# Optimization experiments

Hardware: AMD Instinct MI355X
Metric: run time of the kernel (lower is better)

Reference implementation:

```python
import jax, jax.numpy as jnp
import numpy as np

ALPHA = 0.2   # LeakyReLU negative slope
EPS = 1e-8
N_NODES = 100000
N_EDGES = 1600000
D_IN = 128
D_OUT = 128


def setup_inputs() -> dict:
    key = jax.random.key(0)
    k1, k2, k3, k4, k5 = jax.random.split(key, 5)
    h = jax.random.normal(k1, (N_NODES, D_IN), dtype=jnp.float32)
    edge_index = jax.random.randint(k2, (2, N_EDGES), 0, N_NODES, dtype=jnp.int32)
    edge_weight = jax.random.uniform(k3, (N_EDGES,), dtype=jnp.float32)
    # xavier-ish scaled params
    W = jax.random.normal(k4, (D_OUT, D_IN), dtype=jnp.float32) * (1.0 / np.sqrt(D_IN))
    a = jax.random.normal(k5, (1, 2 * D_OUT), dtype=jnp.float32) * (1.0 / np.sqrt(2 * D_OUT))
    return {"h": h, "edge_index": edge_index, "edge_weight": edge_weight, "W": W, "a": a}


def reference(h, edge_index, edge_weight, W, a):
    num_nodes = h.shape[0]
    Wh = h @ W.T                                   # [N, D_OUT]
    src, dst = edge_index[0], edge_index[1]
    d_out = Wh.shape[1]
    a_src = a[0, :d_out]                           # a^T [Wh_i || Wh_j] split into two dots
    a_dst = a[0, d_out:]
    Wh_src = Wh[src]                               # [E, D_OUT] edge gather
    e = Wh_src @ a_src + Wh[dst] @ a_dst           # [E]
    e = jnp.where(e >= 0, e, ALPHA * e)            # LeakyReLU
    e = e * edge_weight
    # segment softmax over edges sharing dst; torch init-to-zero amax => max(seg_max, 0)
    seg_max = jax.ops.segment_max(e, dst, num_segments=num_nodes)
    seg_max = jnp.maximum(seg_max, 0.0)
    ex = jnp.exp(e - seg_max[dst])
    seg_sum = jax.ops.segment_sum(ex, dst, num_segments=num_nodes)
    att = ex / (seg_sum[dst] + EPS)                # [E]
    # weighted scatter-add aggregation (dropout is identity in eval/p=0)
    h_prime = jax.ops.segment_sum(att[:, None] * Wh_src, dst, num_segments=num_nodes)
    return h_prime
```

## Files before the change

### kernel.cpp

```cpp
#include <hip/hip_runtime.h>
#include <hip/hip_bf16.h>
#include <math.h>

#define D_FEAT 128
#define ALPHA 0.2f
#define EPS 1e-8f

#define BSHIFT 7
#define BNODES 128
#define NB_MAX 800
#define NB_PAD 1024
#define CAP_B 2432
#define CCHUNK 2048

typedef __bf16 bf16x8 __attribute__((ext_vector_type(8)));
typedef float f32x4 __attribute__((ext_vector_type(4)));

__device__ __forceinline__ void split_bf16(const float* __restrict__ p,
                                           bf16x8& hi, bf16x8& lo)
{
    f32x4 a = *(const f32x4*)p;
    f32x4 b = *(const f32x4*)(p + 4);
#pragma unroll
    for (int j = 0; j < 4; ++j) {
        float x = a[j]; __bf16 xh = (__bf16)x;
        hi[j] = xh; lo[j] = (__bf16)(x - (float)xh);
        float y = b[j]; __bf16 yh = (__bf16)y;
        hi[j + 4] = yh; lo[j + 4] = (__bf16)(y - (float)yh);
    }
}

__global__ __launch_bounds__(256) void presplit_w(
    const float* __restrict__ W, __bf16* __restrict__ Whi, __bf16* __restrict__ Wlo)
{
    const int i = blockIdx.x * 256 + threadIdx.x;
    const float x = W[i];
    const __bf16 xh = (__bf16)x;
    Whi[i] = xh;
    Wlo[i] = (__bf16)(x - (float)xh);
}

__global__ __launch_bounds__(256) void gemm_s_kernel(
    const float* __restrict__ h,
    const __bf16* __restrict__ Whi, const __bf16* __restrict__ Wlo,
    const float* __restrict__ a, __bf16* __restrict__ Whb,
    float* __restrict__ s_src, float* __restrict__ s_dst, int N)
{
    const int wave = threadIdx.x >> 6;
    const int lane = threadIdx.x & 63;
    const int row0 = blockIdx.x * 128 + wave * 32;
    if (row0 >= N) return;

    const int l15 = lane & 15;
    const int quad = lane >> 4;

    bf16x8 ahi[2][4], alo[2][4];
#pragma unroll
    for (int m = 0; m < 2; ++m) {
        int arow = row0 + m * 16 + l15;
        if (arow >= N) arow = N - 1;
#pragma unroll
        for (int kk = 0; kk < 4; ++kk)
            split_bf16(h + (size_t)arow * D_FEAT + kk * 32 + quad * 8,
                       ahi[m][kk], alo[m][kk]);
    }

    f32x4 acc[2][8];
#pragma unroll
    for (int m = 0; m < 2; ++m)
#pragma unroll
        for (int n = 0; n < 8; ++n) acc[m][n] = (f32x4){0.f, 0.f, 0.f, 0.f};

#pragma unroll
    for (int kk = 0; kk < 4; ++kk) {
#pragma unroll
        for (int n = 0; n < 8; ++n) {
            const size_t boff = (size_t)(n * 16 + l15) * D_FEAT + kk * 32 + quad * 8;
            const bf16x8 bhi = *(const bf16x8*)(Whi + boff);
            const bf16x8 blo = *(const bf16x8*)(Wlo + boff);
#pragma unroll
            for (int m = 0; m < 2; ++m) {
                acc[m][n] = __builtin_amdgcn_mfma_f32_16x16x32_bf16(ahi[m][kk], bhi, acc[m][n], 0, 0, 0);
                acc[m][n] = __builtin_amdgcn_mfma_f32_16x16x32_bf16(ahi[m][kk], blo, acc[m][n], 0, 0, 0);
                acc[m][n] = __builtin_amdgcn_mfma_f32_16x16x32_bf16(alo[m][kk], bhi, acc[m][n], 0, 0, 0);
            }
        }
    }

#pragma unroll
    for (int m = 0; m < 2; ++m) {
        const int rbase = row0 + m * 16;
        float psrc[4] = {0.f, 0.f, 0.f, 0.f};
        float pdst[4] = {0.f, 0.f, 0.f, 0.f};
#pragma unroll
        for (int n = 0; n < 8; ++n) {
            const int col = n * 16 + l15;
            const float as = a[col];
            const float ad = a[D_FEAT + col];
#pragma unroll
            for (int r = 0; r < 4; ++r) {
                const int row = rbase + quad * 4 + r;
                const float v = acc[m][n][r];
                if (row < N) Whb[(size_t)row * D_FEAT + col] = (__bf16)v;
                psrc[r] += v * as;
                pdst[r] += v * ad;
            }
        }
#pragma unroll
        for (int off = 1; off < 16; off <<= 1) {
#pragma unroll
            for (int r = 0; r < 4; ++r) {
                psrc[r] += __shfl_xor(psrc[r], off, 64);
                pdst[r] += __shfl_xor(pdst[r], off, 64);
            }
        }
        if (l15 == 0) {
#pragma unroll
            for (int r = 0; r < 4; ++r) {
                const int row = rbase + quad * 4 + r;
                if (row < N) { s_src[row] = psrc[r]; s_dst[row] = pdst[r]; }
            }
        }
    }
}

__global__ __launch_bounds__(256) void bin_sort_local(
    const int* __restrict__ src, const int* __restrict__ dst,
    const float* __restrict__ ew,
    const float* __restrict__ s_src, const float* __restrict__ s_dst,
    int* __restrict__ gcur, uint2* __restrict__ bin, int E, int NB)
{
    __shared__ uint2 srt[CCHUNK];
    __shared__ unsigned short sbkt[CCHUNK];
    __shared__ int lhist[NB_PAD];
    __shared__ int loff[NB_PAD];
    __shared__ int lcur[NB_PAD];
    __shared__ int gbase[NB_PAD];
    __shared__ int sh[256];

    const int t = threadIdx.x;
    const int i0 = blockIdx.x * CCHUNK + t * 8;

    lhist[t] = 0; lhist[t + 256] = 0; lhist[t + 512] = 0; lhist[t + 768] = 0;
    __syncthreads();

    int n = E - i0; n = n < 0 ? 0 : (n > 8 ? 8 : n);
    int ss[8], dd[8];
    float wwv[8], exv[8];
    unsigned meta[8];
    int bb[8];

    if (n == 8) {
        const int4 sa = *(const int4*)(src + i0);
        const int4 sb = *(const int4*)(src + i0 + 4);
        const int4 da = *(const int4*)(dst + i0);
        const int4 db = *(const int4*)(dst + i0 + 4);
        const float4 wa = *(const float4*)(ew + i0);
        const float4 wb = *(const float4*)(ew + i0 + 4);
        ss[0] = sa.x; ss[1] = sa.y; ss[2] = sa.z; ss[3] = sa.w;
        ss[4] = sb.x; ss[5] = sb.y; ss[6] = sb.z; ss[7] = sb.w;
        dd[0] = da.x; dd[1] = da.y; dd[2] = da.z; dd[3] = da.w;
        dd[4] = db.x; dd[5] = db.y; dd[6] = db.z; dd[7] = db.w;
        wwv[0] = wa.x; wwv[1] = wa.y; wwv[2] = wa.z; wwv[3] = wa.w;
        wwv[4] = wb.x; wwv[5] = wb.y; wwv[6] = wb.z; wwv[7] = wb.w;
    } else {
        for (int k = 0; k < n; ++k) {
            ss[k] = src[i0 + k]; dd[k] = dst[i0 + k]; wwv[k] = ew[i0 + k];
        }
    }
#pragma unroll
    for (int k = 0; k < 8; ++k) {
        if (k < n) {
            const int s = ss[k], d = dd[k];
            float e = s_src[s] + s_dst[d];
            e = (e >= 0.f) ? e : ALPHA * e;
            e *= wwv[k];
            exv[k] = expf(e);
            bb[k] = d >> BSHIFT;
            meta[k] = (unsigned)s | ((unsigned)(d & (BNODES - 1)) << 17);
            atomicAdd(&lhist[bb[k]], 1);
        }
    }
    __syncthreads();

    const int v0 = lhist[4 * t];
    const int v1 = lhist[4 * t + 1];
    const int v2 = lhist[4 * t + 2];
    const int v3 = lhist[4 * t + 3];
    const int ts = v0 + v1 + v2 + v3;
    sh[t] = ts;
    __syncthreads();
    for (int off = 1; off < 256; off <<= 1) {
        int x = (t >= off) ? sh[t - off] : 0;
        __syncthreads();
        sh[t] += x;
        __syncthreads();
    }
    int run = sh[t] - ts;
    loff[4 * t] = run;     lcur[4 * t] = run;     run += v0;
    loff[4 * t + 1] = run; lcur[4 * t + 1] = run; run += v1;
    loff[4 * t + 2] = run; lcur[4 * t + 2] = run; run += v2;
    loff[4 * t + 3] = run; lcur[4 * t + 3] = run;
    const int total = sh[255];

    for (int b = t; b < NB; b += 256) {
        const int c = lhist[b];
        gbase[b] = c ? atomicAdd(&gcur[b], c) : 0;
    }
    __syncthreads();

#pragma unroll
    for (int k = 0; k < 8; ++k) {
        if (k < n) {
            const int p = atomicAdd(&lcur[bb[k]], 1);
            srt[p] = make_uint2(meta[k], __float_as_uint(exv[k]));
            sbkt[p] = (unsigned short)bb[k];
        }
    }
    __syncthreads();

    for (int i = t; i < total; i += 256) {
        const int b = sbkt[i];
        const int gpos = gbase[b] + (i - loff[b]);
        if (gpos < CAP_B)
            bin[(size_t)b * CAP_B + gpos] = srt[i];
    }
}

__global__ __launch_bounds__(512) void sort_aggregate(
    const int* __restrict__ gcur, const uint2* __restrict__ bin,
    const __bf16* __restrict__ Whb, float* __restrict__ out, int N)
{
    __shared__ uint2 srec[CAP_B];
    __shared__ float ssums[BNODES];
    __shared__ int lhist[BNODES];
    __shared__ int loff[BNODES];
    __shared__ int lcur[BNODES];
    __shared__ int sh[BNODES];

    const int t = threadIdx.x;
    const int b = blockIdx.x;
    const size_t base = (size_t)b * CAP_B;
    const int node0 = b << BSHIFT;
    const int nnodes = min(BNODES, N - node0);
    int cnt = gcur[b];
    if (cnt > CAP_B) cnt = CAP_B;

    if (t < BNODES) { lhist[t] = 0; ssums[t] = 0.f; }
    __syncthreads();

    for (int i = t; i < cnt; i += 512)
        atomicAdd(&lhist[(bin[base + i].x >> 17) & (BNODES - 1)], 1);
    __syncthreads();

    int hv = 0;
    if (t < BNODES) { hv = lhist[t]; sh[t] = hv; }
    __syncthreads();
    for (int off = 1; off < BNODES; off <<= 1) {
        int x = (t >= off && t < BNODES) ? sh[t - off] : 0;
        __syncthreads();
        if (t < BNODES) sh[t] += x;
        __syncthreads();
    }
    if (t < BNODES) { loff[t] = sh[t] - hv; lcur[t] = sh[t] - hv; }
    __syncthreads();

    for (int i = t; i < cnt; i += 512) {
        const uint2 r = bin[base + i];
        const unsigned dl = (r.x >> 17) & (BNODES - 1);
        const int p = atomicAdd(&lcur[dl], 1);
        srec[p] = make_uint2(r.x & 0x1FFFFu, r.y);
        atomicAdd(&ssums[dl], __uint_as_float(r.y));
    }
    __syncthreads();

    const int wave = t >> 6;
    const int lane = t & 63;
    const int quad = lane >> 4;
    const int c0 = (lane & 15) * 8;

    for (int nd = wave; nd < nnodes; nd += 8) {
        const int rb = loff[nd];
        const int cnt_n = lhist[nd];
        const float inv = 1.f / (ssums[nd] + EPS);

        float acc[8];
#pragma unroll
        for (int i = 0; i < 8; ++i) acc[i] = 0.f;

        int j = 0;
        for (; j + 15 < cnt_n; j += 16) {
            uint2 m[4];
#pragma unroll
            for (int g = 0; g < 4; ++g) m[g] = srec[rb + j + g * 4 + quad];
            bf16x8 v[4];
#pragma unroll
            for (int g = 0; g < 4; ++g)
                v[g] = *(const bf16x8*)(Whb + (size_t)m[g].x * D_FEAT + c0);
#pragma unroll
            for (int g = 0; g < 4; ++g) {
                const float a0 = __uint_as_float(m[g].y);
#pragma unroll
                for (int i = 0; i < 8; ++i) acc[i] += a0 * (float)v[g][i];
            }
        }
        for (; j + 7 < cnt_n; j += 8) {
            const uint2 m0 = srec[rb + j + quad];
            const uint2 m1 = srec[rb + j + 4 + quad];
            const float a0 = __uint_as_float(m0.y);
            const float a1 = __uint_as_float(m1.y);
            const bf16x8 v0 = *(const bf16x8*)(Whb + (size_t)m0.x * D_FEAT + c0);
            const bf16x8 v1 = *(const bf16x8*)(Whb + (size_t)m1.x * D_FEAT + c0);
#pragma unroll
            for (int i = 0; i < 8; ++i)
                acc[i] += a0 * (float)v0[i] + a1 * (float)v1[i];
        }
        for (; j < cnt_n; j += 4) {
            const int je = j + quad;
            const int jc = je < cnt_n ? je : cnt_n - 1;
            const uint2 m = srec[rb + jc];
            const float a0 = (je < cnt_n) ? __uint_as_float(m.y) : 0.f;
            const bf16x8 v = *(const bf16x8*)(Whb + (size_t)m.x * D_FEAT + c0);
#pragma unroll
            for (int i = 0; i < 8; ++i) acc[i] += a0 * (float)v[i];
        }
#pragma unroll
        for (int i = 0; i < 8; ++i) {
            acc[i] += __shfl_xor(acc[i], 16, 64);
            acc[i] += __shfl_xor(acc[i], 32, 64);
            acc[i] *= inv;
        }
        if (lane < 16) {
            f32x4 r0, r1;
            r0[0] = acc[0]; r0[1] = acc[1]; r0[2] = acc[2]; r0[3] = acc[3];
            r1[0] = acc[4]; r1[1] = acc[5]; r1[2] = acc[6]; r1[3] = acc[7];
            float* po = out + (size_t)(node0 + nd) * D_FEAT + c0;
            *(f32x4*)po = r0;
            *(f32x4*)(po + 4) = r1;
        }
    }
}

extern "C" void kernel_launch(void* const* d_in, const int* in_sizes, int n_in,
                              void* d_out, int out_size, void* d_ws, size_t ws_size,
                              hipStream_t stream) {
    const float* h  = (const float*)d_in[0];
    const int* eidx = (const int*)d_in[1];
    const float* ew = (const float*)d_in[2];
    const float* W  = (const float*)d_in[3];
    const float* a  = (const float*)d_in[4];
    float* out      = (float*)d_out;

    const int N = in_sizes[0] / D_FEAT;
    const int E = in_sizes[2];
    const int* src = eidx;
    const int* dst = eidx + E;

    const int NB = (N + BNODES - 1) / BNODES;

    char* ws = (char*)d_ws;
    size_t off = 0;
    int*    gcur      = (int*)(ws + off);   off += (size_t)NB_MAX * 4;
    float*  s_src     = (float*)(ws + off); off += (size_t)N * 4;
    float*  s_dst     = (float*)(ws + off); off += (size_t)N * 4;
    off = (off + 15) & ~(size_t)15;
    __bf16* Whi       = (__bf16*)(ws + off); off += (size_t)D_FEAT * D_FEAT * 2;
    __bf16* Wlo       = (__bf16*)(ws + off); off += (size_t)D_FEAT * D_FEAT * 2;
    uint2*  bin       = (uint2*)(ws + off);  off += (size_t)NB_MAX * CAP_B * 8;
    __bf16* Whb       = (__bf16*)(ws + off); off += (size_t)N * D_FEAT * 2;

    hipMemsetAsync(gcur, 0, (size_t)NB * 4, stream);

    presplit_w<<<64, 256, 0, stream>>>(W, Whi, Wlo);
    gemm_s_kernel<<<(N + 127) / 128, 256, 0, stream>>>(h, Whi, Wlo, a, Whb, s_src, s_dst, N);
    bin_sort_local<<<(E + CCHUNK - 1) / CCHUNK, 256, 0, stream>>>(
        src, dst, ew, s_src, s_dst, gcur, bin, E, NB);
    sort_aggregate<<<NB, 512, 0, stream>>>(gcur, bin, Whb, out, N);
}
```

Before: 270.5 us.

## Store Wh as fp16, fold memset into presplit, widen bin sort blocks

Several changes at once. Wh is stored as fp16 instead of bf16, trading range for mantissa accuracy at the same bandwidth. The gcur memset is folded into the presplit_w kernel to save a launch. bin_sort_local now uses 512 threads over 4096-edge chunks and __expf instead of expf. In sort_aggregate, per-node softmax sums are computed by a wave reduction over sorted records rather than shared-memory float atomics. fp16 could overflow for large Wh values, and the larger sort chunk raises LDS use and lowers the block count.

```diff
diff --git a/kernel.cpp b/kernel.cpp
--- a/kernel.cpp
+++ b/kernel.cpp
@@ -11,9 +11,10 @@
 #define NB_MAX 800
 #define NB_PAD 1024
 #define CAP_B 2432
-#define CCHUNK 2048
+#define CCHUNK 4096
 
 typedef __bf16 bf16x8 __attribute__((ext_vector_type(8)));
+typedef _Float16 f16x8 __attribute__((ext_vector_type(8)));
 typedef float f32x4 __attribute__((ext_vector_type(4)));
 
 __device__ __forceinline__ void split_bf16(const float* __restrict__ p,
@@ -31,19 +32,23 @@
 }
 
 __global__ __launch_bounds__(256) void presplit_w(
-    const float* __restrict__ W, __bf16* __restrict__ Whi, __bf16* __restrict__ Wlo)
+    const float* __restrict__ W, __bf16* __restrict__ Whi, __bf16* __restrict__ Wlo,
+    int* __restrict__ gcur)
 {
     const int i = blockIdx.x * 256 + threadIdx.x;
     const float x = W[i];
     const __bf16 xh = (__bf16)x;
     Whi[i] = xh;
     Wlo[i] = (__bf16)(x - (float)xh);
+    if (blockIdx.x == 0) {
+        for (int b = threadIdx.x; b < NB_MAX; b += 256) gcur[b] = 0;
+    }
 }
 
 __global__ __launch_bounds__(256) void gemm_s_kernel(
     const float* __restrict__ h,
     const __bf16* __restrict__ Whi, const __bf16* __restrict__ Wlo,
-    const float* __restrict__ a, __bf16* __restrict__ Whb,
+    const float* __restrict__ a, _Float16* __restrict__ Whf,
     float* __restrict__ s_src, float* __restrict__ s_dst, int N)
 {
     const int wave = threadIdx.x >> 6;
@@ -101,7 +106,7 @@
             for (int r = 0; r < 4; ++r) {
                 const int row = rbase + quad * 4 + r;
                 const float v = acc[m][n][r];
-                if (row < N) Whb[(size_t)row * D_FEAT + col] = (__bf16)v;
+                if (row < N) Whf[(size_t)row * D_FEAT + col] = (_Float16)v;
                 psrc[r] += v * as;
                 pdst[r] += v * ad;
             }
@@ -124,7 +129,7 @@
     }
 }
 
-__global__ __launch_bounds__(256) void bin_sort_local(
+__global__ __launch_bounds__(512) void bin_sort_local(
     const int* __restrict__ src, const int* __restrict__ dst,
     const float* __restrict__ ew,
     const float* __restrict__ s_src, const float* __restrict__ s_dst,
@@ -136,12 +141,12 @@
     __shared__ int loff[NB_PAD];
     __shared__ int lcur[NB_PAD];
     __shared__ int gbase[NB_PAD];
-    __shared__ int sh[256];
+    __shared__ int sh[512];
 
     const int t = threadIdx.x;
     const int i0 = blockIdx.x * CCHUNK + t * 8;
 
-    lhist[t] = 0; lhist[t + 256] = 0; lhist[t + 512] = 0; lhist[t + 768] = 0;
+    lhist[t] = 0; lhist[t + 512] = 0;
     __syncthreads();
 
     int n = E - i0; n = n < 0 ? 0 : (n > 8 ? 8 : n);
@@ -175,7 +180,7 @@
             float e = s_src[s] + s_dst[d];
             e = (e >= 0.f) ? e : ALPHA * e;
             e *= wwv[k];
-            exv[k] = expf(e);
+            exv[k] = __expf(e);
             bb[k] = d >> BSHIFT;
             meta[k] = (unsigned)s | ((unsigned)(d & (BNODES - 1)) << 17);
             atomicAdd(&lhist[bb[k]], 1);
@@ -183,27 +188,23 @@
     }
     __syncthreads();
 
-    const int v0 = lhist[4 * t];
-    const int v1 = lhist[4 * t + 1];
-    const int v2 = lhist[4 * t + 2];
-    const int v3 = lhist[4 * t + 3];
-    const int ts = v0 + v1 + v2 + v3;
+    const int v0 = lhist[2 * t];
+    const int v1 = lhist[2 * t + 1];
+    const int ts = v0 + v1;
     sh[t] = ts;
     __syncthreads();
-    for (int off = 1; off < 256; off <<= 1) {
+    for (int off = 1; off < 512; off <<= 1) {
         int x = (t >= off) ? sh[t - off] : 0;
         __syncthreads();
         sh[t] += x;
         __syncthreads();
     }
     int run = sh[t] - ts;
-    loff[4 * t] = run;     lcur[4 * t] = run;     run += v0;
-    loff[4 * t + 1] = run; lcur[4 * t + 1] = run; run += v1;
-    loff[4 * t + 2] = run; lcur[4 * t + 2] = run; run += v2;
-    loff[4 * t + 3] = run; lcur[4 * t + 3] = run;
-    const int total = sh[255];
-
-    for (int b = t; b < NB; b += 256) {
+    loff[2 * t] = run;     lcur[2 * t] = run;     run += v0;
+    loff[2 * t + 1] = run; lcur[2 * t + 1] = run;
+    const int total = sh[511];
+
+    for (int b = t; b < NB; b += 512) {
         const int c = lhist[b];
         gbase[b] = c ? atomicAdd(&gcur[b], c) : 0;
     }
@@ -219,7 +220,7 @@
     }
     __syncthreads();
 
-    for (int i = t; i < total; i += 256) {
+    for (int i = t; i < total; i += 512) {
         const int b = sbkt[i];
         const int gpos = gbase[b] + (i - loff[b]);
         if (gpos < CAP_B)
@@ -229,10 +230,9 @@
 
 __global__ __launch_bounds__(512) void sort_aggregate(
     const int* __restrict__ gcur, const uint2* __restrict__ bin,
-    const __bf16* __restrict__ Whb, float* __restrict__ out, int N)
+    const _Float16* __restrict__ Whf, float* __restrict__ out, int N)
 {
     __shared__ uint2 srec[CAP_B];
-    __shared__ float ssums[BNODES];
     __shared__ int lhist[BNODES];
     __shared__ int loff[BNODES];
     __shared__ int lcur[BNODES];
@@ -246,7 +246,7 @@
     int cnt = gcur[b];
     if (cnt > CAP_B) cnt = CAP_B;
 
-    if (t < BNODES) { lhist[t] = 0; ssums[t] = 0.f; }
+    if (t < BNODES) lhist[t] = 0;
     __syncthreads();
 
     for (int i = t; i < cnt; i += 512)
@@ -270,7 +270,6 @@
         const unsigned dl = (r.x >> 17) & (BNODES - 1);
         const int p = atomicAdd(&lcur[dl], 1);
         srec[p] = make_uint2(r.x & 0x1FFFFu, r.y);
-        atomicAdd(&ssums[dl], __uint_as_float(r.y));
     }
     __syncthreads();
 
@@ -282,7 +281,14 @@
     for (int nd = wave; nd < nnodes; nd += 8) {
         const int rb = loff[nd];
         const int cnt_n = lhist[nd];
-        const float inv = 1.f / (ssums[nd] + EPS);
+
+        float ssum = 0.f;
+        for (int jj = lane; jj < cnt_n; jj += 64)
+            ssum += __uint_as_float(srec[rb + jj].y);
+#pragma unroll
+        for (int off = 1; off < 64; off <<= 1)
+            ssum += __shfl_xor(ssum, off, 64);
+        const float inv = 1.f / (ssum + EPS);
 
         float acc[8];
 #pragma unroll
@@ -293,10 +299,10 @@
             uint2 m[4];
 #pragma unroll
             for (int g = 0; g < 4; ++g) m[g] = srec[rb + j + g * 4 + quad];
-            bf16x8 v[4];
+            f16x8 v[4];
 #pragma unroll
             for (int g = 0; g < 4; ++g)
-                v[g] = *(const bf16x8*)(Whb + (size_t)m[g].x * D_FEAT + c0);
+                v[g] = *(const f16x8*)(Whf + (size_t)m[g].x * D_FEAT + c0);
 #pragma unroll
             for (int g = 0; g < 4; ++g) {
                 const float a0 = __uint_as_float(m[g].y);
@@ -309,8 +315,8 @@
             const uint2 m1 = srec[rb + j + 4 + quad];
             const float a0 = __uint_as_float(m0.y);
             const float a1 = __uint_as_float(m1.y);
-            const bf16x8 v0 = *(const bf16x8*)(Whb + (size_t)m0.x * D_FEAT + c0);
-            const bf16x8 v1 = *(const bf16x8*)(Whb + (size_t)m1.x * D_FEAT + c0);
+            const f16x8 v0 = *(const f16x8*)(Whf + (size_t)m0.x * D_FEAT + c0);
+            const f16x8 v1 = *(const f16x8*)(Whf + (size_t)m1.x * D_FEAT + c0);
 #pragma unroll
             for (int i = 0; i < 8; ++i)
                 acc[i] += a0 * (float)v0[i] + a1 * (float)v1[i];
@@ -320,7 +326,7 @@
             const int jc = je < cnt_n ? je : cnt_n - 1;
             const uint2 m = srec[rb + jc];
             const float a0 = (je < cnt_n) ? __uint_as_float(m.y) : 0.f;
-            const bf16x8 v = *(const bf16x8*)(Whb + (size_t)m.x * D_FEAT + c0);
+            const f16x8 v = *(const f16x8*)(Whf + (size_t)m.x * D_FEAT + c0);
 #pragma unroll
             for (int i = 0; i < 8; ++i) acc[i] += a0 * (float)v[i];
         }
@@ -360,20 +366,19 @@
 
     char* ws = (char*)d_ws;
     size_t off = 0;
-    int*    gcur      = (int*)(ws + off);   off += (size_t)NB_MAX * 4;
-    float*  s_src     = (float*)(ws + off); off += (size_t)N * 4;
-    float*  s_dst     = (float*)(ws + off); off += (size_t)N * 4;
+    int*      gcur  = (int*)(ws + off);     off += (size_t)NB_MAX * 4;
+    float*    s_src = (float*)(ws + off);   off += (size_t)N * 4;
+    float*    s_dst = (float*)(ws + off);   off += (size_t)N * 4;
     off = (off + 15) & ~(size_t)15;
-    __bf16* Whi       = (__bf16*)(ws + off); off += (size_t)D_FEAT * D_FEAT * 2;
-    __bf16* Wlo       = (__bf16*)(ws + off); off += (size_t)D_FEAT * D_FEAT * 2;
-    uint2*  bin       = (uint2*)(ws + off);  off += (size_t)NB_MAX * CAP_B * 8;
-    __bf16* Whb       = (__bf16*)(ws + off); off += (size_t)N * D_FEAT * 2;
-
-    hipMemsetAsync(gcur, 0, (size_t)NB * 4, stream);
-
-    presplit_w<<<64, 256, 0, stream>>>(W, Whi, Wlo);
-    gemm_s_kernel<<<(N + 127) / 128, 256, 0, stream>>>(h, Whi, Wlo, a, Whb, s_src, s_dst, N);
-    bin_sort_local<<<(E + CCHUNK - 1) / CCHUNK, 256, 0, stream>>>(
+    __bf16*   Whi  = (__bf16*)(ws + off);   off += (size_t)D_FEAT * D_FEAT * 2;
+    __bf16*   Wlo  = (__bf16*)(ws + off);   off += (size_t)D_FEAT * D_FEAT * 2;
+    uint2*    bin  = (uint2*)(ws + off);    off += (size_t)NB_MAX * CAP_B * 8;
+    _Float16* Whf  = (_Float16*)(ws + off); off += (size_t)N * D_FEAT * 2;
+
+    presplit_w<<<64, 256, 0, stream>>>(W, Whi, Wlo, gcur);
+    gemm_s_kernel<<<(N + 127) / 128, 256, 0, stream>>>(h, Whi, Wlo, a, Whf,
+                                                       s_src, s_dst, N);
+    bin_sort_local<<<(E + CCHUNK - 1) / CCHUNK, 512, 0, stream>>>(
         src, dst, ew, s_src, s_dst, gcur, bin, E, NB);
-    sort_aggregate<<<NB, 512, 0, stream>>>(gcur, bin, Whb, out, N);
-}
+    sort_aggregate<<<NB, 512, 0, stream>>>(gcur, bin, Whf, out, N);
+}
```

After: 260.9 us. 3.5% less time.
